# Kernel optimization log

Measured on AMD Instinct MI355X. Metric: run time of the kernel, lower is better.

## Reference

```python
import jax, jax.numpy as jnp
import numpy as np

K2 = 4.0 / 3.0; K4 = 4.10451; K5 = 19.08857; K6 = 254.5553148552
KN = 7.5; WF = 6.0; GA = 3.0; GC = 2.0
BOHR = 0.5291772105638411; HARTREE = 27.211386024367243
C2BOHR = 1.0 / BOHR; C2EV = 0.5 * HARTREE
N_ATOMS = 50000; N_NEIGH = 48; ZMAX = 87; NREF = 7; NFREQ = 23; KCN = 7


def _sp_inv(x):
    # softplus_inverse
    return jnp.float32(np.log(np.expm1(x)))


def setup_inputs() -> dict:
    key = jax.random.key(0)
    ks = jax.random.split(key, 24)
    P = N_ATOMS * N_NEIGH
    u = lambda k, shp, lo, hi: jax.random.uniform(k, shp, jnp.float32, lo, hi)
    Z = jax.random.randint(ks[0], (N_ATOMS,), 0, ZMAX)
    idx_i = jnp.repeat(jnp.arange(N_ATOMS), N_NEIGH)  # center index per pair
    idx_j = jax.random.randint(ks[1], (P,), 0, N_ATOMS)
    r_ij = u(ks[2], (P,), 1.5, 6.0)  # Angstrom
    qa = 0.05 * jax.random.normal(ks[3], (N_ATOMS,), jnp.float32)
    return dict(
        Z=Z, idx_i=idx_i, idx_j=idx_j, r_ij=r_ij, qa=qa,
        s6_raw=_sp_inv(1.0), s8_raw=_sp_inv(1.61679827),
        a1_raw=_sp_inv(0.44959224), a2_raw=_sp_inv(3.35743605),
        scaleq_raw=_sp_inv(1.0),
        refsys=jax.random.randint(ks[4], (ZMAX, NREF), 0, ZMAX),
        zeff=u(ks[5], (ZMAX,), 1.0, 10.0),
        refh=u(ks[6], (ZMAX, NREF), 0.0, 0.3),
        sscale=u(ks[7], (ZMAX,), 0.5, 1.5),
        secaiw=u(ks[8], (ZMAX, NFREQ), 0.0, 1.0),
        gam=u(ks[9], (ZMAX,), 0.05, 0.5),
        ascale=u(ks[10], (ZMAX, NREF), 0.5, 1.5),
        alphaiw=u(ks[11], (ZMAX, NREF, NFREQ), 0.0, 5.0),
        hcount=u(ks[12], (ZMAX, NREF), 0.0, 2.0),
        casimir_polder_weights=u(ks[13], (NFREQ,), 0.0, 0.5),
        rcov=u(ks[14], (ZMAX,), 0.6, 2.5),
        en=u(ks[15], (ZMAX,), 0.5, 4.0),
        ncount_mask=(u(ks[16], (ZMAX, NREF, KCN), 0.0, 1.0) < 0.6).astype(jnp.float32),
        ncount_weight=u(ks[17], (ZMAX, NREF, KCN), 0.5, 2.0),
        cn=u(ks[18], (ZMAX, NREF, KCN), 0.0, 6.0),
        fixgweights=(lambda g: g / jnp.sum(g, -1, keepdims=True))(u(ks[19], (ZMAX, NREF), 0.1, 1.0)),
        refq=u(ks[20], (ZMAX, NREF), -0.2, 0.2),
        sqrt_r4r2=u(ks[21], (ZMAX,), 1.0, 4.0),
    )


def compute_refc6(scaleq, refsys, zeff, refh, sscale, secaiw, gam, ascale, alphaiw, hcount, cpw):
    iz = zeff[refsys]                                   # [Z, nref]
    qref = iz
    qmod = iz + refh * scaleq
    qmod_ = jnp.where(qmod > 1e-8, qmod, 1.0)
    zeta = jnp.where(qmod > 1e-8,
                     jnp.exp(GA * (1.0 - jnp.exp(gam[refsys] * GC * (1.0 - qref / qmod_)))),
                     np.exp(GA).astype(np.float32))
    asec = sscale[refsys][..., None] * secaiw[refsys] * zeta[..., None]  # [Z,nref,nfreq]
    alpha = jnp.maximum(ascale[..., None] * (alphaiw - hcount[..., None] * asec), 0.0)
    return (3.0 / np.pi) * jnp.einsum('iax,jbx,x->ijab', alpha, alpha, cpw)  # [Z,Z,nref,nref]


def reference(Z, idx_i, idx_j, r_ij, qa, s6_raw, s8_raw, a1_raw, a2_raw, scaleq_raw,
              refsys, zeff, refh, sscale, secaiw, gam, ascale, alphaiw, hcount,
              casimir_polder_weights, rcov, en, ncount_mask, ncount_weight, cn,
              fixgweights, refq, sqrt_r4r2):
    n_atoms = qa.shape[0]
    scaleq = jax.nn.softplus(scaleq_raw)
    # refc6 is computed under no_grad in the original module
    refc6 = jax.lax.stop_gradient(compute_refc6(scaleq, refsys, zeff, refh, sscale,
                                                secaiw, gam, ascale, alphaiw, hcount,
                                                casimir_polder_weights))
    r = r_ij * C2BOHR
    Zi = Z[idx_i]; Zj = Z[idx_j]
    # coordination-number contribution per pair, scattered to centers
    rco = K2 * (rcov[Zi] + rcov[Zj])
    den = K4 * jnp.exp(-(jnp.abs(en[Zi] - en[Zj]) + K5) ** 2 / K6)
    tmp = den * 0.5 * (1.0 + jax.lax.erf(-KN * (r - rco) / rco))
    covcn = jax.ops.segment_sum(tmp, idx_i, num_segments=n_atoms)
    # gaussian reference-CN weights [n_atoms, nref]
    gweights = jnp.sum(ncount_mask[Z] * jnp.exp(-WF * ncount_weight[Z] * (covcn[:, None, None] - cn[Z]) ** 2), -1)
    norm = jnp.sum(gweights, -1, keepdims=True)
    gweights = jnp.where(norm > 1e-8, gweights / jnp.where(norm > 1e-8, norm, 1.0), fixgweights[Z])
    # charge scaling zeta [n_atoms, nref]
    iz = zeff[Z][:, None]
    qref = iz + refq[Z] * scaleq
    qmod = iz + qa[:, None]
    qmod_ = jnp.where(qmod > 1e-8, qmod, 1.0)
    zeta = jnp.where(qmod > 1e-8,
                     jnp.exp(GA * (1.0 - jnp.exp(gam[Z][:, None] * GC * (1.0 - qref / qmod_)))),
                     np.exp(GA).astype(np.float32)) * gweights
    zetai = zeta[idx_i]; zetaj = zeta[idx_j]            # [P, nref]
    refc6ij = refc6[Zi, Zj]                             # [P, nref, nref]
    c6ij = jnp.einsum('pab,pa,pb->p', refc6ij, zetai, zetaj)
    r4r2ij = np.float32(np.sqrt(3.0)) * sqrt_r4r2[Zi] * sqrt_r4r2[Zj]
    a1 = jax.nn.softplus(a1_raw); a2 = jax.nn.softplus(a2_raw)
    r0 = a1 * r4r2ij + a2
    oor6 = 1.0 / (r ** 6 + r0 ** 6)
    oor8 = 1.0 / (r ** 8 + r0 ** 8)
    s6 = jax.nn.softplus(s6_raw); s8 = jax.nn.softplus(s8_raw)
    edisp = -c6ij * (s6 * oor6 + s8 * r4r2ij ** 2 * oor8) * C2EV
    eatom = jax.ops.segment_sum(edisp, idx_i, num_segments=n_atoms)
    zeros = jnp.zeros((n_atoms,), r_ij.dtype)  # compute_atomic_quantities=False
    return (eatom, zeros, zeros)
```

## Files before the change

kernel.cpp:

```cpp
#include <hip/hip_runtime.h>
#include <hip/hip_fp16.h>
#include <math.h>

#define NATOMS 50000
#define NNEIGH 48
#define ZMAXV 87
#define NREFV 7
#define NFREQV 23
#define KCNV 7
#define XPAD 24
#define XPADH 32
#define APB 8
#define TPB 192
#define PPB (APB * NNEIGH)

#define C2BOHR 1.8897261258369282f
#define C2EV 13.605693012183622f
#define K2C 1.33333333333333333f
#define K4C 4.10451f
#define K5C 19.08857f
#define K6INV (1.0f / 254.5553148552f)
#define KNC 7.5f
#define EXP_GA 20.085536923187668f
#define QRT3 1.3160740129524924f

__device__ __forceinline__ float sp(float x) { return log1pf(expf(x)); }

__global__ __launch_bounds__(256) void k_setup(
    const int* __restrict__ Z, const int* __restrict__ refsys,
    const float* __restrict__ zeff, const float* __restrict__ refh,
    const float* __restrict__ sscale, const float* __restrict__ secaiw,
    const float* __restrict__ gam, const float* __restrict__ ascale,
    const float* __restrict__ alphaiw, const float* __restrict__ hcount,
    const float* __restrict__ rcov, const float* __restrict__ en,
    const float* __restrict__ s6r, const float* __restrict__ s8r,
    const float* __restrict__ a1r, const float* __restrict__ a2r,
    const float* __restrict__ sqr,
    float* __restrict__ scal_out, float* __restrict__ alpha_out,
    float2* __restrict__ re2_out, float* __restrict__ zero_out)
{
    int e = blockIdx.x * 256 + threadIdx.x;
    if (e == 0) {
        scal_out[0] = sp(s6r[0]);
        scal_out[1] = sp(s8r[0]);
        scal_out[2] = sp(a1r[0]);
        scal_out[3] = sp(a2r[0]);
    }
    if (e < 2 * NATOMS) zero_out[e] = 0.0f;
    if (e < NATOMS) {
        int z = Z[e];
        re2_out[e] = make_float2(rcov[z], en[z]);
    }
    if (e < ZMAXV * NREFV * XPAD) {
        int x = e % XPAD;
        int za = e / XPAD;
        float v = 0.0f;
        if (x < NFREQV) {
            float scaleq = sp(sqr[0]);
            int rs = refsys[za];
            float iz = zeff[rs];
            float qmod = iz + refh[za] * scaleq;
            float zeta = (qmod > 1e-8f)
                ? __expf(3.0f * (1.0f - __expf(gam[rs] * 2.0f * (1.0f - iz / qmod))))
                : EXP_GA;
            float asec = sscale[rs] * secaiw[rs * NFREQV + x] * zeta;
            v = fmaxf(ascale[za] * (alphaiw[za * NFREQV + x] - hcount[za] * asec), 0.0f);
        }
        alpha_out[e] = v;
    }
}

__global__ __launch_bounds__(TPB) void k_atoms(
    const int* __restrict__ Z, const int* __restrict__ idx_j,
    const float* __restrict__ r_ij, const float* __restrict__ qa,
    const float* __restrict__ sqr, const float* __restrict__ zeff,
    const float* __restrict__ gam, const float2* __restrict__ re2,
    const float* __restrict__ nmask, const float* __restrict__ nweight,
    const float* __restrict__ cn, const float* __restrict__ fixg,
    const float* __restrict__ refq, const float* __restrict__ cpw,
    const float* __restrict__ alpha_tab, const float* __restrict__ sr4r2,
    __half2* __restrict__ A_out2)
{
    __shared__ float sh[PPB];
    __shared__ float covcn[APB];
    __shared__ float gwl[APB][NREFV];
    __shared__ float ztl[APB][NREFV];
    const int t = threadIdx.x;
    const int a0 = blockIdx.x * APB;

    {
        int p0 = blockIdx.x * PPB + t;
        int p1 = p0 + TPB;
        int al0 = t / NNEIGH;
        int j0 = idx_j[p0];
        int j1 = idx_j[p1];
        float rr0 = r_ij[p0];
        float rr1 = r_ij[p1];
        float2 rej0 = re2[j0];
        float2 rej1 = re2[j1];
        float2 rei0 = re2[a0 + al0];
        float2 rei1 = re2[a0 + al0 + 4];

        float r0 = rr0 * C2BOHR;
        float rco0 = K2C * (rei0.x + rej0.x);
        float d0 = fabsf(rei0.y - rej0.y) + K5C;
        float den0 = K4C * __expf(-d0 * d0 * K6INV);
        sh[t] = den0 * 0.5f * (1.0f + erff(-KNC * (r0 - rco0) / rco0));

        float r1 = rr1 * C2BOHR;
        float rco1 = K2C * (rei1.x + rej1.x);
        float d1 = fabsf(rei1.y - rej1.y) + K5C;
        float den1 = K4C * __expf(-d1 * d1 * K6INV);
        sh[t + TPB] = den1 * 0.5f * (1.0f + erff(-KNC * (r1 - rco1) / rco1));
    }
    __syncthreads();
    if (t < APB) {
        float s = 0.0f;
        for (int k = 0; k < NNEIGH; k++) s += sh[t * NNEIGH + k];
        covcn[t] = s;
    }
    __syncthreads();

    if (t < APB * NREFV) {
        int al = t / NREFV, a = t % NREFV;
        int zl = Z[a0 + al];
        float cc = covcn[al];
        const float* mB = nmask + (zl * NREFV + a) * KCNV;
        const float* wB = nweight + (zl * NREFV + a) * KCNV;
        const float* cB = cn + (zl * NREFV + a) * KCNV;
        float g = 0.0f;
        for (int k = 0; k < KCNV; k++) {
            float dc = cc - cB[k];
            g += mB[k] * __expf(-6.0f * wB[k] * dc * dc);
        }
        gwl[al][a] = g;
    }
    __syncthreads();

    if (t < APB * NREFV) {
        int al = t / NREFV, a = t % NREFV;
        int zl = Z[a0 + al];
        float norm = 0.0f;
        for (int b = 0; b < NREFV; b++) norm += gwl[al][b];
        float w = (norm > 1e-8f) ? (gwl[al][a] / norm) : fixg[zl * NREFV + a];
        float scaleq = sp(sqr[0]);
        float iz = zeff[zl];
        float qref = iz + refq[zl * NREFV + a] * scaleq;
        float qmod = iz + qa[a0 + al];
        float zeta = (qmod > 1e-8f)
            ? __expf(3.0f * (1.0f - __expf(gam[zl] * 2.0f * (1.0f - qref / qmod))))
            : EXP_GA;
        ztl[al][a] = zeta * w;
    }
    __syncthreads();

    if (t < APB * (XPADH / 2)) {
        int al = t >> 4, xh = t & 15;
        int x0 = 2 * xh, x1 = 2 * xh + 1;
        int zl = Z[a0 + al];
        float v0 = 0.0f, v1 = 0.0f;
        if (x0 < NFREQV) {
            float s = 0.0f;
            #pragma unroll
            for (int a = 0; a < NREFV; a++)
                s += ztl[al][a] * alpha_tab[(zl * NREFV + a) * XPAD + x0];
            v0 = s * sqrtf(cpw[x0] * 0.9549296585513721f);
        }
        if (x1 < NFREQV) {
            float s = 0.0f;
            #pragma unroll
            for (int a = 0; a < NREFV; a++)
                s += ztl[al][a] * alpha_tab[(zl * NREFV + a) * XPAD + x1];
            v1 = s * sqrtf(cpw[x1] * 0.9549296585513721f);
        } else if (x1 == NFREQV) {
            v1 = QRT3 * sr4r2[zl];
        }
        A_out2[(size_t)(a0 + al) * (XPADH / 2) + xh] = __floats2half2_rn(v0, v1);
    }
}

__global__ __launch_bounds__(TPB) void k_pairs(
    const int* __restrict__ idx_j, const float* __restrict__ r_ij,
    const float* __restrict__ scal, const __half* __restrict__ Ah,
    float* __restrict__ eatom)
{
    __shared__ float sh[PPB];
    __shared__ float Ai[APB][NFREQV];
    __shared__ float Asi[APB];
    const int t = threadIdx.x;
    const int a0 = blockIdx.x * APB;

    {
        int al = t / XPAD, x = t - al * XPAD;
        float v = __half2float(Ah[(size_t)(a0 + al) * XPADH + x]);
        if (x < NFREQV) Ai[al][x] = v;
        else Asi[al] = v;
    }
    __syncthreads();

    const float s6 = scal[0], s8 = scal[1], a1 = scal[2], a2 = scal[3];

    int p0 = blockIdx.x * PPB + t;
    int p1 = p0 + TPB;
    int al0 = t / NNEIGH;
    int al1 = al0 + 4;
    int j0 = idx_j[p0];
    int j1 = idx_j[p1];
    float rr0 = r_ij[p0];
    float rr1 = r_ij[p1];

    const float4* P0 = (const float4*)(Ah + (size_t)j0 * XPADH);
    const float4* P1 = (const float4*)(Ah + (size_t)j1 * XPADH);
    float4 u0 = P0[0], u1 = P0[1], u2 = P0[2];
    float4 w0 = P1[0], w1 = P1[1], w2 = P1[2];

    float c60 = 0.0f, c61 = 0.0f, sj0, sj1;
    {
        const __half2* hu = (const __half2*)&u0;
        const __half2* a2p[3] = { (const __half2*)&u0, (const __half2*)&u1, (const __half2*)&u2 };
        const __half2* b2p[3] = { (const __half2*)&w0, (const __half2*)&w1, (const __half2*)&w2 };
        (void)hu;
        #pragma unroll
        for (int seg = 0; seg < 3; seg++) {
            #pragma unroll
            for (int k = 0; k < 4; k++) {
                int x = seg * 8 + 2 * k;
                float2 fa = __half22float2(a2p[seg][k]);
                float2 fb = __half22float2(b2p[seg][k]);
                if (x < NFREQV)      c60 += fa.x * Ai[al0][x];
                else                 sj0 = fa.x;
                if (x + 1 < NFREQV)  c60 += fa.y * Ai[al0][x + 1];
                else if (x + 1 == NFREQV) sj0 = fa.y;
                if (x < NFREQV)      c61 += fb.x * Ai[al1][x];
                if (x + 1 < NFREQV)  c61 += fb.y * Ai[al1][x + 1];
                else if (x + 1 == NFREQV) sj1 = fb.y;
            }
        }
    }

    float e0, e1;
    {
        float r = rr0 * C2BOHR;
        float r4r2 = Asi[al0] * sj0;
        float r0v = a1 * r4r2 + a2;
        float r2 = r * r, r4 = r2 * r2, r6 = r4 * r2, r8 = r4 * r4;
        float p2 = r0v * r0v, p4 = p2 * p2, p6 = p4 * p2, p8 = p4 * p4;
        e0 = -c60 * (s6 / (r6 + p6) + s8 * r4r2 * r4r2 / (r8 + p8)) * C2EV;
    }
    {
        float r = rr1 * C2BOHR;
        float r4r2 = Asi[al1] * sj1;
        float r0v = a1 * r4r2 + a2;
        float r2 = r * r, r4 = r2 * r2, r6 = r4 * r2, r8 = r4 * r4;
        float p2 = r0v * r0v, p4 = p2 * p2, p6 = p4 * p2, p8 = p4 * p4;
        e1 = -c61 * (s6 / (r6 + p6) + s8 * r4r2 * r4r2 / (r8 + p8)) * C2EV;
    }

    sh[t] = e0;
    sh[t + TPB] = e1;
    __syncthreads();
    if (t < APB) {
        float s = 0.0f;
        for (int k = 0; k < NNEIGH; k++) s += sh[t * NNEIGH + k];
        eatom[a0 + t] = s;
    }
}

extern "C" void kernel_launch(void* const* d_in, const int* in_sizes, int n_in,
                              void* d_out, int out_size, void* d_ws, size_t ws_size,
                              hipStream_t stream)
{
    const int*   Z       = (const int*)  d_in[0];
    const int*   idx_j   = (const int*)  d_in[2];
    const float* r_ij    = (const float*)d_in[3];
    const float* qa      = (const float*)d_in[4];
    const float* s6r     = (const float*)d_in[5];
    const float* s8r     = (const float*)d_in[6];
    const float* a1r     = (const float*)d_in[7];
    const float* a2r     = (const float*)d_in[8];
    const float* sqraw   = (const float*)d_in[9];
    const int*   refsys  = (const int*)  d_in[10];
    const float* zeff    = (const float*)d_in[11];
    const float* refh    = (const float*)d_in[12];
    const float* sscale  = (const float*)d_in[13];
    const float* secaiw  = (const float*)d_in[14];
    const float* gam     = (const float*)d_in[15];
    const float* ascale  = (const float*)d_in[16];
    const float* alphaiw = (const float*)d_in[17];
    const float* hcount  = (const float*)d_in[18];
    const float* cpw     = (const float*)d_in[19];
    const float* rcov    = (const float*)d_in[20];
    const float* en      = (const float*)d_in[21];
    const float* nmask   = (const float*)d_in[22];
    const float* nweight = (const float*)d_in[23];
    const float* cn      = (const float*)d_in[24];
    const float* fixg    = (const float*)d_in[25];
    const float* refq    = (const float*)d_in[26];
    const float* sr4r2   = (const float*)d_in[27];

    char* wsb = (char*)d_ws;
    float*  scal  = (float*)(wsb);
    float*  alpha = (float*)(wsb + 64);
    float2* re2   = (float2*)(wsb + 58528);
    __half* Ah    = (__half*)(wsb + 458752);

    float* eatom = (float*)d_out;
    float* zeros = eatom + NATOMS;

    k_setup<<<391, 256, 0, stream>>>(Z, refsys, zeff, refh, sscale, secaiw, gam,
                                     ascale, alphaiw, hcount, rcov, en,
                                     s6r, s8r, a1r, a2r, sqraw,
                                     scal, alpha, re2, zeros);
    k_atoms<<<NATOMS / APB, TPB, 0, stream>>>(
        Z, idx_j, r_ij, qa, sqraw, zeff, gam, re2,
        nmask, nweight, cn, fixg, refq, cpw, alpha, sr4r2, (__half2*)Ah);
    k_pairs<<<NATOMS / APB, TPB, 0, stream>>>(
        idx_j, r_ij, scal, Ah, eatom);
}
```

Before: 180.1 us.

## Remap pair threads per atom, use fast erf, nontemporal loads, precompute scaleq

Replaces erff with an Abramowitz-Stegun polynomial approximation plus __expf, and remaps threads so each handles two neighbours of the same atom. This halves the shared-memory reduction length and removes the separate al0/al1 indexing. Pair inputs are read with nontemporal loads, and softplus(scaleq) is computed once in the setup kernel instead of per thread. The erf approximation adds an error of roughly 1e-7 in absolute terms.

```diff
diff --git a/kernel.cpp b/kernel.cpp
--- a/kernel.cpp
+++ b/kernel.cpp
@@ -25,6 +25,15 @@
 #define QRT3 1.3160740129524924f
 
 __device__ __forceinline__ float sp(float x) { return log1pf(expf(x)); }
+
+__device__ __forceinline__ float fast_erf(float x) {
+    float ax = fabsf(x);
+    float t = 1.0f / fmaf(0.3275911f, ax, 1.0f);
+    float poly = t * fmaf(t, fmaf(t, fmaf(t, fmaf(t, 1.061405429f, -1.453152027f),
+                                          1.421413741f), -0.284496736f), 0.254829592f);
+    float y = 1.0f - poly * __expf(-ax * ax);
+    return copysignf(y, x);
+}
 
 __global__ __launch_bounds__(256) void k_setup(
     const int* __restrict__ Z, const int* __restrict__ refsys,
@@ -45,6 +54,7 @@
         scal_out[1] = sp(s8r[0]);
         scal_out[2] = sp(a1r[0]);
         scal_out[3] = sp(a2r[0]);
+        scal_out[4] = sp(sqr[0]);
     }
     if (e < 2 * NATOMS) zero_out[e] = 0.0f;
     if (e < NATOMS) {
@@ -73,7 +83,7 @@
 __global__ __launch_bounds__(TPB) void k_atoms(
     const int* __restrict__ Z, const int* __restrict__ idx_j,
     const float* __restrict__ r_ij, const float* __restrict__ qa,
-    const float* __restrict__ sqr, const float* __restrict__ zeff,
+    const float* __restrict__ scal, const float* __restrict__ zeff,
     const float* __restrict__ gam, const float2* __restrict__ re2,
     const float* __restrict__ nmask, const float* __restrict__ nweight,
     const float* __restrict__ cn, const float* __restrict__ fixg,
@@ -81,50 +91,52 @@
     const float* __restrict__ alpha_tab, const float* __restrict__ sr4r2,
     __half2* __restrict__ A_out2)
 {
-    __shared__ float sh[PPB];
+    __shared__ float sh[TPB];
     __shared__ float covcn[APB];
     __shared__ float gwl[APB][NREFV];
     __shared__ float ztl[APB][NREFV];
     const int t = threadIdx.x;
     const int a0 = blockIdx.x * APB;
-
-    {
-        int p0 = blockIdx.x * PPB + t;
-        int p1 = p0 + TPB;
-        int al0 = t / NNEIGH;
-        int j0 = idx_j[p0];
-        int j1 = idx_j[p1];
-        float rr0 = r_ij[p0];
-        float rr1 = r_ij[p1];
+    const int al = t / 24;
+    const int kk = t - al * 24;
+
+    {
+        int p0 = blockIdx.x * PPB + al * NNEIGH + kk;
+        int p1 = p0 + 24;
+        int j0 = __builtin_nontemporal_load(idx_j + p0);
+        int j1 = __builtin_nontemporal_load(idx_j + p1);
+        float rr0 = __builtin_nontemporal_load(r_ij + p0);
+        float rr1 = __builtin_nontemporal_load(r_ij + p1);
         float2 rej0 = re2[j0];
         float2 rej1 = re2[j1];
-        float2 rei0 = re2[a0 + al0];
-        float2 rei1 = re2[a0 + al0 + 4];
+        float2 rei = re2[a0 + al];
 
         float r0 = rr0 * C2BOHR;
-        float rco0 = K2C * (rei0.x + rej0.x);
-        float d0 = fabsf(rei0.y - rej0.y) + K5C;
+        float rco0 = K2C * (rei.x + rej0.x);
+        float d0 = fabsf(rei.y - rej0.y) + K5C;
         float den0 = K4C * __expf(-d0 * d0 * K6INV);
-        sh[t] = den0 * 0.5f * (1.0f + erff(-KNC * (r0 - rco0) / rco0));
+        float t0 = den0 * 0.5f * (1.0f + fast_erf(-KNC * (r0 - rco0) / rco0));
 
         float r1 = rr1 * C2BOHR;
-        float rco1 = K2C * (rei1.x + rej1.x);
-        float d1 = fabsf(rei1.y - rej1.y) + K5C;
+        float rco1 = K2C * (rei.x + rej1.x);
+        float d1 = fabsf(rei.y - rej1.y) + K5C;
         float den1 = K4C * __expf(-d1 * d1 * K6INV);
-        sh[t + TPB] = den1 * 0.5f * (1.0f + erff(-KNC * (r1 - rco1) / rco1));
+        float t1 = den1 * 0.5f * (1.0f + fast_erf(-KNC * (r1 - rco1) / rco1));
+
+        sh[t] = t0 + t1;
     }
     __syncthreads();
     if (t < APB) {
         float s = 0.0f;
-        for (int k = 0; k < NNEIGH; k++) s += sh[t * NNEIGH + k];
+        for (int k = 0; k < 24; k++) s += sh[t * 24 + k];
         covcn[t] = s;
     }
     __syncthreads();
 
     if (t < APB * NREFV) {
-        int al = t / NREFV, a = t % NREFV;
-        int zl = Z[a0 + al];
-        float cc = covcn[al];
+        int a_l = t / NREFV, a = t % NREFV;
+        int zl = Z[a0 + a_l];
+        float cc = covcn[a_l];
         const float* mB = nmask + (zl * NREFV + a) * KCNV;
         const float* wB = nweight + (zl * NREFV + a) * KCNV;
         const float* cB = cn + (zl * NREFV + a) * KCNV;
@@ -133,49 +145,49 @@
             float dc = cc - cB[k];
             g += mB[k] * __expf(-6.0f * wB[k] * dc * dc);
         }
-        gwl[al][a] = g;
+        gwl[a_l][a] = g;
     }
     __syncthreads();
 
     if (t < APB * NREFV) {
-        int al = t / NREFV, a = t % NREFV;
-        int zl = Z[a0 + al];
+        int a_l = t / NREFV, a = t % NREFV;
+        int zl = Z[a0 + a_l];
         float norm = 0.0f;
-        for (int b = 0; b < NREFV; b++) norm += gwl[al][b];
-        float w = (norm > 1e-8f) ? (gwl[al][a] / norm) : fixg[zl * NREFV + a];
-        float scaleq = sp(sqr[0]);
+        for (int b = 0; b < NREFV; b++) norm += gwl[a_l][b];
+        float w = (norm > 1e-8f) ? (gwl[a_l][a] / norm) : fixg[zl * NREFV + a];
+        float scaleq = scal[4];
         float iz = zeff[zl];
         float qref = iz + refq[zl * NREFV + a] * scaleq;
-        float qmod = iz + qa[a0 + al];
+        float qmod = iz + qa[a0 + a_l];
         float zeta = (qmod > 1e-8f)
             ? __expf(3.0f * (1.0f - __expf(gam[zl] * 2.0f * (1.0f - qref / qmod))))
             : EXP_GA;
-        ztl[al][a] = zeta * w;
+        ztl[a_l][a] = zeta * w;
     }
     __syncthreads();
 
     if (t < APB * (XPADH / 2)) {
-        int al = t >> 4, xh = t & 15;
+        int a_l = t >> 4, xh = t & 15;
         int x0 = 2 * xh, x1 = 2 * xh + 1;
-        int zl = Z[a0 + al];
+        int zl = Z[a0 + a_l];
         float v0 = 0.0f, v1 = 0.0f;
         if (x0 < NFREQV) {
             float s = 0.0f;
             #pragma unroll
             for (int a = 0; a < NREFV; a++)
-                s += ztl[al][a] * alpha_tab[(zl * NREFV + a) * XPAD + x0];
+                s += ztl[a_l][a] * alpha_tab[(zl * NREFV + a) * XPAD + x0];
             v0 = s * sqrtf(cpw[x0] * 0.9549296585513721f);
         }
         if (x1 < NFREQV) {
             float s = 0.0f;
             #pragma unroll
             for (int a = 0; a < NREFV; a++)
-                s += ztl[al][a] * alpha_tab[(zl * NREFV + a) * XPAD + x1];
+                s += ztl[a_l][a] * alpha_tab[(zl * NREFV + a) * XPAD + x1];
             v1 = s * sqrtf(cpw[x1] * 0.9549296585513721f);
         } else if (x1 == NFREQV) {
             v1 = QRT3 * sr4r2[zl];
         }
-        A_out2[(size_t)(a0 + al) * (XPADH / 2) + xh] = __floats2half2_rn(v0, v1);
+        A_out2[(size_t)(a0 + a_l) * (XPADH / 2) + xh] = __floats2half2_rn(v0, v1);
     }
 }
 
@@ -184,42 +196,39 @@
     const float* __restrict__ scal, const __half* __restrict__ Ah,
     float* __restrict__ eatom)
 {
-    __shared__ float sh[PPB];
+    __shared__ float sh[TPB];
     __shared__ float Ai[APB][NFREQV];
     __shared__ float Asi[APB];
     const int t = threadIdx.x;
     const int a0 = blockIdx.x * APB;
-
-    {
-        int al = t / XPAD, x = t - al * XPAD;
-        float v = __half2float(Ah[(size_t)(a0 + al) * XPADH + x]);
-        if (x < NFREQV) Ai[al][x] = v;
+    const int al = t / 24;
+    const int kk = t - al * 24;
+
+    {
+        float v = __half2float(Ah[(size_t)(a0 + al) * XPADH + kk]);
+        if (kk < NFREQV) Ai[al][kk] = v;
         else Asi[al] = v;
     }
     __syncthreads();
 
     const float s6 = scal[0], s8 = scal[1], a1 = scal[2], a2 = scal[3];
 
-    int p0 = blockIdx.x * PPB + t;
-    int p1 = p0 + TPB;
-    int al0 = t / NNEIGH;
-    int al1 = al0 + 4;
-    int j0 = idx_j[p0];
-    int j1 = idx_j[p1];
-    float rr0 = r_ij[p0];
-    float rr1 = r_ij[p1];
+    int p0 = blockIdx.x * PPB + al * NNEIGH + kk;
+    int p1 = p0 + 24;
+    int j0 = __builtin_nontemporal_load(idx_j + p0);
+    int j1 = __builtin_nontemporal_load(idx_j + p1);
+    float rr0 = __builtin_nontemporal_load(r_ij + p0);
+    float rr1 = __builtin_nontemporal_load(r_ij + p1);
 
     const float4* P0 = (const float4*)(Ah + (size_t)j0 * XPADH);
     const float4* P1 = (const float4*)(Ah + (size_t)j1 * XPADH);
     float4 u0 = P0[0], u1 = P0[1], u2 = P0[2];
     float4 w0 = P1[0], w1 = P1[1], w2 = P1[2];
 
-    float c60 = 0.0f, c61 = 0.0f, sj0, sj1;
-    {
-        const __half2* hu = (const __half2*)&u0;
+    float c60 = 0.0f, c61 = 0.0f, sj0 = 0.0f, sj1 = 0.0f;
+    {
         const __half2* a2p[3] = { (const __half2*)&u0, (const __half2*)&u1, (const __half2*)&u2 };
         const __half2* b2p[3] = { (const __half2*)&w0, (const __half2*)&w1, (const __half2*)&w2 };
-        (void)hu;
         #pragma unroll
         for (int seg = 0; seg < 3; seg++) {
             #pragma unroll
@@ -227,13 +236,9 @@
                 int x = seg * 8 + 2 * k;
                 float2 fa = __half22float2(a2p[seg][k]);
                 float2 fb = __half22float2(b2p[seg][k]);
-                if (x < NFREQV)      c60 += fa.x * Ai[al0][x];
-                else                 sj0 = fa.x;
-                if (x + 1 < NFREQV)  c60 += fa.y * Ai[al0][x + 1];
-                else if (x + 1 == NFREQV) sj0 = fa.y;
-                if (x < NFREQV)      c61 += fb.x * Ai[al1][x];
-                if (x + 1 < NFREQV)  c61 += fb.y * Ai[al1][x + 1];
-                else if (x + 1 == NFREQV) sj1 = fb.y;
+                if (x < NFREQV) { c60 += fa.x * Ai[al][x]; c61 += fb.x * Ai[al][x]; }
+                if (x + 1 < NFREQV) { c60 += fa.y * Ai[al][x + 1]; c61 += fb.y * Ai[al][x + 1]; }
+                else if (x + 1 == NFREQV) { sj0 = fa.y; sj1 = fb.y; }
             }
         }
     }
@@ -241,7 +246,7 @@
     float e0, e1;
     {
         float r = rr0 * C2BOHR;
-        float r4r2 = Asi[al0] * sj0;
+        float r4r2 = Asi[al] * sj0;
         float r0v = a1 * r4r2 + a2;
         float r2 = r * r, r4 = r2 * r2, r6 = r4 * r2, r8 = r4 * r4;
         float p2 = r0v * r0v, p4 = p2 * p2, p6 = p4 * p2, p8 = p4 * p4;
@@ -249,19 +254,18 @@
     }
     {
         float r = rr1 * C2BOHR;
-        float r4r2 = Asi[al1] * sj1;
+        float r4r2 = Asi[al] * sj1;
         float r0v = a1 * r4r2 + a2;
         float r2 = r * r, r4 = r2 * r2, r6 = r4 * r2, r8 = r4 * r4;
         float p2 = r0v * r0v, p4 = p2 * p2, p6 = p4 * p2, p8 = p4 * p4;
         e1 = -c61 * (s6 / (r6 + p6) + s8 * r4r2 * r4r2 / (r8 + p8)) * C2EV;
     }
 
-    sh[t] = e0;
-    sh[t + TPB] = e1;
+    sh[t] = e0 + e1;
     __syncthreads();
     if (t < APB) {
         float s = 0.0f;
-        for (int k = 0; k < NNEIGH; k++) s += sh[t * NNEIGH + k];
+        for (int k = 0; k < 24; k++) s += sh[t * 24 + k];
         eatom[a0 + t] = s;
     }
 }
@@ -312,7 +316,7 @@
                                      s6r, s8r, a1r, a2r, sqraw,
                                      scal, alpha, re2, zeros);
     k_atoms<<<NATOMS / APB, TPB, 0, stream>>>(
-        Z, idx_j, r_ij, qa, sqraw, zeff, gam, re2,
+        Z, idx_j, r_ij, qa, scal, zeff, gam, re2,
         nmask, nweight, cn, fixg, refq, cpw, alpha, sr4r2, (__half2*)Ah);
     k_pairs<<<NATOMS / APB, TPB, 0, stream>>>(
         idx_j, r_ij, scal, Ah, eatom);
```

After: 186.5 us. 1.04x slower.
